# Kernel optimization log

Hardware: AMD Instinct MI355X
Metric: run time of the kernel (lower is better)

## Reference

```python
import jax, jax.numpy as jnp
import numpy as np


def _gnn_layer(feat, W, b, src, dst, n_nodes):
    # edge-wise: gather src feats -> Linear -> scatter-sum at dst
    m = feat @ W + b                                   # [N, out]
    agg = jax.ops.segment_sum(m[src], dst, num_segments=n_nodes)  # [N, out]
    # concat aggregated messages with self-transformed features -> 2*out
    return jnp.concatenate([agg, m], axis=-1)


def setup_inputs() -> dict:
    key = jax.random.key(0)
    ks = jax.random.split(key, 6)
    N, E, D_IN, D_OUT = 50000, 800000, 128, 128
    features = jax.random.normal(ks[0], (N, D_IN), dtype=jnp.float32)
    src = jax.random.randint(ks[1], (E,), 0, N, dtype=jnp.int32)
    dst = jax.random.randint(ks[2], (E,), 0, N, dtype=jnp.int32)
    W1 = jax.random.normal(ks[3], (D_IN, D_OUT), dtype=jnp.float32) / np.sqrt(D_IN)
    b1 = jnp.zeros((D_OUT,), dtype=jnp.float32)
    W2 = jax.random.normal(ks[4], (2 * D_OUT, D_OUT), dtype=jnp.float32) / np.sqrt(2 * D_OUT)
    b2 = jnp.zeros((D_OUT,), dtype=jnp.float32)
    return {"features": features, "src": src, "dst": dst,
            "W1": W1, "b1": b1, "W2": W2, "b2": b2}


def reference(features, src, dst, W1, b1, W2, b2):
    n_nodes = features.shape[0]
    feat = _gnn_layer(features, W1, b1, src, dst, n_nodes)  # [N, 2*out]
    feat = _gnn_layer(feat, W2, b2, src, dst, n_nodes)      # [N, 2*out]
    return feat
```

## Files before the change

### kernel.cpp

```cpp
#include <hip/hip_runtime.h>


#define D 128
#define CBLK 256
#define DCAP 6144

typedef __attribute__((ext_vector_type(8))) short short8;
typedef __attribute__((ext_vector_type(4))) float float4v;
typedef unsigned short ushort_t;
typedef unsigned int uint_t;

static __device__ __forceinline__ ushort_t f2bf(float f) {
    uint_t u = __builtin_bit_cast(uint_t, f);
    u += 0x7FFFu + ((u >> 16) & 1u);
    return (ushort_t)(u >> 16);
}
static __device__ __forceinline__ float bfhi(uint_t u) {
    return __builtin_bit_cast(float, u & 0xFFFF0000u);
}
static __device__ __forceinline__ float bflo(uint_t u) {
    return __builtin_bit_cast(float, u << 16);
}

static __device__ __forceinline__ void gemm1_body(
    const float* __restrict__ X, const ushort_t* __restrict__ Wp,
    const float* __restrict__ bias, ushort_t* __restrict__ Ybf,
    int N, int gb)
{
    const int wave = threadIdx.x >> 6;
    const int lane = threadIdx.x & 63;
    const int quad = lane >> 4;
    const int l16  = lane & 15;
    const int r0   = gb * 64 + wave * 16;

    float4v acc[8];
    #pragma unroll
    for (int cg = 0; cg < 8; ++cg) {
        float bv = bias[cg * 16 + l16];
        float4v b4 = {bv, bv, bv, bv};
        acc[cg] = b4;
    }

    const short8* wp8 = (const short8*)Wp;

    #pragma unroll
    for (int kb = 0; kb < 4; ++kb) {
        const int k0 = kb * 32 + quad * 8;
        int row = r0 + l16;
        if (row >= N) row = N - 1;
        const float* p = &X[(size_t)row * D + k0];
        float4 x0 = *(const float4*)p;
        float4 x1 = *(const float4*)(p + 4);
        short8 a;
        a[0] = (short)f2bf(x0.x); a[1] = (short)f2bf(x0.y);
        a[2] = (short)f2bf(x0.z); a[3] = (short)f2bf(x0.w);
        a[4] = (short)f2bf(x1.x); a[5] = (short)f2bf(x1.y);
        a[6] = (short)f2bf(x1.z); a[7] = (short)f2bf(x1.w);
        #pragma unroll
        for (int cg = 0; cg < 8; ++cg) {
            short8 b = wp8[(kb * 8 + cg) * 64 + lane];
            acc[cg] = __builtin_amdgcn_mfma_f32_16x16x32_bf16(a, b, acc[cg], 0, 0, 0);
        }
    }

    const int rowb = r0 + quad * 4;
    #pragma unroll
    for (int cg = 0; cg < 8; ++cg) {
        int col = cg * 16 + l16;
        #pragma unroll
        for (int i = 0; i < 4; ++i) {
            int row = rowb + i;
            if (row < N) Ybf[(size_t)row * D + col] = f2bf(acc[cg][i]);
        }
    }
}

__global__ __launch_bounds__(256) void packw_binA(
    const float* __restrict__ W1, const float* __restrict__ W2,
    ushort_t* __restrict__ W1p, ushort_t* __restrict__ W2p,
    const int* __restrict__ dst, int* __restrict__ mat, int E, int NB)
{
    __shared__ int h[256];
    if (blockIdx.x < CBLK) {
        const int c = blockIdx.x;
        for (int i = threadIdx.x; i < NB; i += 256) h[i] = 0;
        __syncthreads();
        const int chunk = (E + CBLK - 1) / CBLK;
        int e0 = c * chunk, e1 = e0 + chunk; if (e1 > E) e1 = E;
        for (int e = e0 + threadIdx.x; e < e1; e += 256)
            atomicAdd(&h[dst[e] >> 8], 1);
        __syncthreads();
        for (int i = threadIdx.x; i < NB; i += 256)
            mat[i * CBLK + c] = h[i];
        return;
    }
    const int n1 = 4 * 8 * 64;
    const int n2 = 8 * 8 * 64;
    int t = (blockIdx.x - CBLK) * 256 + threadIdx.x;
    if (t >= n1 + n2) return;
    const float* W; ushort_t* Wp; int tt;
    if (t < n1) { W = W1; Wp = W1p; tt = t; }
    else        { W = W2; Wp = W2p; tt = t - n1; }
    int lane = tt & 63, cg = (tt >> 6) & 7, kb = tt >> 9;
    int krow = kb * 32 + (lane >> 4) * 8;
    int col  = cg * 16 + (lane & 15);
    #pragma unroll
    for (int j = 0; j < 8; ++j)
        Wp[(size_t)tt * 8 + j] = f2bf(W[(size_t)(krow + j) * D + col]);
}

__global__ __launch_bounds__(256) void binB(
    const int* __restrict__ mat, int* __restrict__ matc,
    int* __restrict__ bb, int* __restrict__ offs, int E, int N, int NB)
{
    __shared__ int s[256];
    __shared__ int ex[256];
    const int b = blockIdx.x;
    const int tid = threadIdx.x;

    int v = 0;
    if (tid < NB) {
        const int* row = &mat[tid * CBLK];
        for (int c = 0; c < CBLK; ++c) v += row[c];
    }
    s[tid] = v; __syncthreads();
    for (int o = 1; o < 256; o <<= 1) {
        int t = (tid >= o) ? s[tid - o] : 0;
        __syncthreads();
        s[tid] += t;
        __syncthreads();
    }
    ex[tid] = s[tid] - v;
    __syncthreads();
    if (b == 0) {
        if (tid < NB) bb[tid] = ex[tid];
        if (tid == 0) { bb[NB] = E; offs[N] = E; }
    }
    const int bbb = ex[b];

    int v2 = mat[b * CBLK + tid];
    __syncthreads();
    s[tid] = v2; __syncthreads();
    for (int o = 1; o < 256; o <<= 1) {
        int t = (tid >= o) ? s[tid - o] : 0;
        __syncthreads();
        s[tid] += t;
        __syncthreads();
    }
    matc[b * CBLK + tid] = bbb + s[tid] - v2;
}

__global__ __launch_bounds__(256) void binC_gemm1(
    const int* __restrict__ src, const int* __restrict__ dst,
    const int* __restrict__ matc, int2* __restrict__ tmp, int E, int NB,
    const float* __restrict__ X, const ushort_t* __restrict__ Wp,
    const float* __restrict__ bias, ushort_t* __restrict__ Ybf, int N)
{
    __shared__ int base[256];
    __shared__ int lcnt[256];
    if (blockIdx.x < CBLK) {
        const int c = blockIdx.x;
        for (int i = threadIdx.x; i < NB; i += 256) {
            base[i] = matc[i * CBLK + c];
            lcnt[i] = 0;
        }
        __syncthreads();
        const int chunk = (E + CBLK - 1) / CBLK;
        int e0 = c * chunk, e1 = e0 + chunk; if (e1 > E) e1 = E;
        for (int e = e0 + threadIdx.x; e < e1; e += 256) {
            int d = dst[e];
            int b = d >> 8;
            int p = base[b] + atomicAdd(&lcnt[b], 1);
            int2 pr; pr.x = d; pr.y = src[e];
            tmp[p] = pr;
        }
        return;
    }
    gemm1_body(X, Wp, bias, Ybf, N, blockIdx.x - CBLK);
}

__global__ __launch_bounds__(256) void binD_gemm1(
    const int2* __restrict__ tmp, const int* __restrict__ bb,
    int* __restrict__ offs, int* __restrict__ bsrc, int N, int NB,
    const float* __restrict__ X, const ushort_t* __restrict__ Wp,
    const float* __restrict__ bias, ushort_t* __restrict__ Ybf, int gb0)
{
    __shared__ int hist[256];
    __shared__ int foff[256];
    __shared__ int cntf[256];
    __shared__ int outS[DCAP];
    if (blockIdx.x >= (uint_t)NB) {
        gemm1_body(X, Wp, bias, Ybf, N, blockIdx.x - NB + gb0);
        return;
    }
    const int b = blockIdx.x;
    const int tid = threadIdx.x;
    const int beg = bb[b], end = bb[b + 1];
    const int cnt = end - beg;
    const int n0 = b << 8;

    hist[tid] = 0;
    __syncthreads();
    for (int i = tid; i < cnt; i += 256)
        atomicAdd(&hist[tmp[beg + i].x & 255], 1);
    __syncthreads();
    int v = hist[tid];
    __syncthreads();
    hist[tid] = v; __syncthreads();
    for (int o = 1; o < 256; o <<= 1) {
        int t = (tid >= o) ? hist[tid - o] : 0;
        __syncthreads();
        hist[tid] += t;
        __syncthreads();
    }
    foff[tid] = hist[tid] - v;
    cntf[tid] = 0;
    __syncthreads();

    int node = n0 + tid;
    if (node < N) offs[node] = beg + foff[tid];

    if (cnt <= DCAP) {
        for (int i = tid; i < cnt; i += 256) {
            int2 p = tmp[beg + i];
            int f = p.x & 255;
            int pos = foff[f] + atomicAdd(&cntf[f], 1);
            outS[pos] = p.y;
        }
        __syncthreads();
        for (int i = tid; i < cnt; i += 256)
            bsrc[beg + i] = outS[i];
    } else {
        for (int i = tid; i < cnt; i += 256) {
            int2 p = tmp[beg + i];
            int f = p.x & 255;
            int pos = foff[f] + atomicAdd(&cntf[f], 1);
            bsrc[beg + pos] = p.y;
        }
    }
}

__global__ __launch_bounds__(256) void gemm2_mfma(
    const ushort_t* __restrict__ A0, const ushort_t* __restrict__ A1,
    const ushort_t* __restrict__ Wp, const float* __restrict__ bias,
    float* __restrict__ Yf, ushort_t* __restrict__ Ybf, int N)
{
    const int wave = threadIdx.x >> 6;
    const int lane = threadIdx.x & 63;
    const int quad = lane >> 4;
    const int l16  = lane & 15;
    const int r0   = blockIdx.x * 64 + wave * 16;

    float4v acc[8];
    #pragma unroll
    for (int cg = 0; cg < 8; ++cg) {
        float bv = bias[cg * 16 + l16];
        float4v b4 = {bv, bv, bv, bv};
        acc[cg] = b4;
    }

    const short8* wp8 = (const short8*)Wp;

    #pragma unroll
    for (int kb = 0; kb < 8; ++kb) {
        const ushort_t* __restrict__ A = (kb < 4) ? A0 : A1;
        const int k0 = (kb & 3) * 32 + quad * 8;
        int row = r0 + l16;
        if (row >= N) row = N - 1;
        short8 a = *(const short8*)&A[(size_t)row * D + k0];
        #pragma unroll
        for (int cg = 0; cg < 8; ++cg) {
            short8 b = wp8[(kb * 8 + cg) * 64 + lane];
            acc[cg] = __builtin_amdgcn_mfma_f32_16x16x32_bf16(a, b, acc[cg], 0, 0, 0);
        }
    }

    const int rowb = r0 + quad * 4;
    #pragma unroll
    for (int cg = 0; cg < 8; ++cg) {
        int col = cg * 16 + l16;
        #pragma unroll
        for (int i = 0; i < 4; ++i) {
            int row = rowb + i;
            if (row < N) {
                float v = acc[cg][i];
                Yf[(size_t)row * 256 + col] = v;
                Ybf[(size_t)row * D + col] = f2bf(v);
            }
        }
    }
}

__global__ __launch_bounds__(256) void gather_bf(
    const ushort_t* __restrict__ msg,
    const int* __restrict__ offs, const int* __restrict__ bsrc,
    ushort_t* __restrict__ aggB,
    float* __restrict__ aggF,
    int N)
{
    int node = (blockIdx.x * 256 + threadIdx.x) >> 6;
    int lane = threadIdx.x & 63;
    if (node >= N) return;
    const int quad = lane >> 4;
    const int c16  = lane & 15;
    int beg = offs[node], end = offs[node + 1];

    float ax[4] = {0.f, 0.f, 0.f, 0.f};
    float ay[4] = {0.f, 0.f, 0.f, 0.f};
    const uint4* mp = (const uint4*)msg;

    for (int base = beg; base < end; base += 64) {
        int cnt = end - base; if (cnt > 64) cnt = 64;
        int sidx = bsrc[base + (lane < cnt ? lane : cnt - 1)];
        for (int j0 = 0; j0 < cnt; j0 += 16) {
            #pragma unroll
            for (int t = 0; t < 4; ++t) {
                int e  = j0 + t * 4 + quad;
                int ec = (e < cnt) ? e : cnt - 1;
                int s  = __shfl(sidx, ec, 64);
                uint4 u = mp[(size_t)s * 16 + c16];
                if (e < cnt) {
                    ax[0] += bflo(u.x); ay[0] += bfhi(u.x);
                    ax[1] += bflo(u.y); ay[1] += bfhi(u.y);
                    ax[2] += bflo(u.z); ay[2] += bfhi(u.z);
                    ax[3] += bflo(u.w); ay[3] += bfhi(u.w);
                }
            }
        }
    }

    #pragma unroll
    for (int k = 0; k < 4; ++k) {
        ax[k] += __shfl_xor(ax[k], 16, 64);
        ax[k] += __shfl_xor(ax[k], 32, 64);
        ay[k] += __shfl_xor(ay[k], 16, 64);
        ay[k] += __shfl_xor(ay[k], 32, 64);
    }

    if (quad == 0) {
        if (aggB) {
            uint4 o;
            o.x = (uint_t)f2bf(ax[0]) | ((uint_t)f2bf(ay[0]) << 16);
            o.y = (uint_t)f2bf(ax[1]) | ((uint_t)f2bf(ay[1]) << 16);
            o.z = (uint_t)f2bf(ax[2]) | ((uint_t)f2bf(ay[2]) << 16);
            o.w = (uint_t)f2bf(ax[3]) | ((uint_t)f2bf(ay[3]) << 16);
            ((uint4*)aggB)[(size_t)node * 16 + c16] = o;
        } else {
            float4 w0 = {ax[0], ay[0], ax[1], ay[1]};
            float4 w1 = {ax[2], ay[2], ax[3], ay[3]};
            float* p = &aggF[(size_t)node * 256 + c16 * 8];
            *(float4*)p = w0;
            *(float4*)(p + 4) = w1;
        }
    }
}

extern "C" void kernel_launch(void* const* d_in, const int* in_sizes, int n_in,
                              void* d_out, int out_size, void* d_ws, size_t ws_size,
                              hipStream_t stream) {
    const float* features = (const float*)d_in[0];
    const int*   src      = (const int*)d_in[1];
    const int*   dst      = (const int*)d_in[2];
    const float* W1       = (const float*)d_in[3];
    const float* b1       = (const float*)d_in[4];
    const float* W2       = (const float*)d_in[5];
    const float* b2       = (const float*)d_in[6];
    float* out = (float*)d_out;

    const int N = in_sizes[0] / D;
    const int E = in_sizes[1];
    const int NB = (N + 255) >> 8;

    ushort_t* m1bf   = (ushort_t*)d_ws;
    ushort_t* agg1bf = m1bf + (size_t)N * D;
    ushort_t* m2bf   = agg1bf + (size_t)N * D;
    ushort_t* W1p    = m2bf + (size_t)N * D;
    ushort_t* W2p    = W1p + 16384;
    int*  mat  = (int*)(W2p + 32768);
    int*  matc = mat + (size_t)NB * CBLK;
    int*  bb   = matc + (size_t)NB * CBLK;
    int*  offs = bb + NB + 1;
    int2* tmp  = (int2*)(offs + N + 1);
    int*  bsrc = (int*)(tmp + (size_t)E);

    const int gemmBlocks = (N + 63) / 64;
    const int gbA = (gemmBlocks * 3) / 5;

    packw_binA<<<CBLK + 24, 256, 0, stream>>>(W1, W2, W1p, W2p, dst, mat, E, NB);
    binB<<<NB, 256, 0, stream>>>(mat, matc, bb, offs, E, N, NB);
    binC_gemm1<<<CBLK + gbA, 256, 0, stream>>>(src, dst, matc, tmp, E, NB,
                                               features, W1p, b1, m1bf, N);
    binD_gemm1<<<NB + (gemmBlocks - gbA), 256, 0, stream>>>(
        tmp, bb, offs, bsrc, N, NB, features, W1p, b1, m1bf, gbA);
    gather_bf<<<(N * 64 + 255) / 256, 256, 0, stream>>>(m1bf, offs, bsrc,
                                                        agg1bf, nullptr, N);
    gemm2_mfma<<<gemmBlocks, 256, 0, stream>>>(agg1bf, m1bf, W2p, b2,
                                               out + D, m2bf, N);
    gather_bf<<<(N * 64 + 255) / 256, 256, 0, stream>>>(m2bf, offs, bsrc,
                                                        nullptr, out, N);
}
```

Measured before the change: 205.5 us.

## Split bin-D scatter across four blocks per bin and double bin-C chunk count

Each destination bin in the second-pass sort is now handled by four blocks. Every block redundantly builds per-quarter histograms so it can compute its own starting offsets, then scatters only its quarter of the edges directly to global memory; the shared-memory staging buffer is dropped. CBLK goes from 256 to 512 so the counting and binning passes use more chunks, with binB scanning pairs to match, and the GEMM split between the two fused kernels is rebalanced. The aim is more parallelism in the sort phases, at the cost of each bin's tmp segment being read four extra times for the histograms and of uncoalesced global writes.

Result: slower. 215.4 us (+4.9%).

```diff
diff --git a/kernel.cpp b/kernel.cpp
--- a/kernel.cpp
+++ b/kernel.cpp
@@ -2,8 +2,7 @@
 
 
 #define D 128
-#define CBLK 256
-#define DCAP 6144
+#define CBLK 512
 
 typedef __attribute__((ext_vector_type(8))) short short8;
 typedef __attribute__((ext_vector_type(4))) float float4v;
@@ -138,16 +137,20 @@
     }
     const int bbb = ex[b];
 
-    int v2 = mat[b * CBLK + tid];
+    int v0 = mat[b * CBLK + 2 * tid];
+    int v1 = mat[b * CBLK + 2 * tid + 1];
+    int pair = v0 + v1;
     __syncthreads();
-    s[tid] = v2; __syncthreads();
+    s[tid] = pair; __syncthreads();
     for (int o = 1; o < 256; o <<= 1) {
         int t = (tid >= o) ? s[tid - o] : 0;
         __syncthreads();
         s[tid] += t;
         __syncthreads();
     }
-    matc[b * CBLK + tid] = bbb + s[tid] - v2;
+    int base = s[tid] - pair;
+    matc[b * CBLK + 2 * tid]     = bbb + base;
+    matc[b * CBLK + 2 * tid + 1] = bbb + base + v0;
 }
 
 __global__ __launch_bounds__(256) void binC_gemm1(
@@ -185,58 +188,59 @@
     const float* __restrict__ X, const ushort_t* __restrict__ Wp,
     const float* __restrict__ bias, ushort_t* __restrict__ Ybf, int gb0)
 {
-    __shared__ int hist[256];
+    __shared__ int h[4][256];
+    __shared__ int sc[256];
     __shared__ int foff[256];
     __shared__ int cntf[256];
-    __shared__ int outS[DCAP];
-    if (blockIdx.x >= (uint_t)NB) {
-        gemm1_body(X, Wp, bias, Ybf, N, blockIdx.x - NB + gb0);
+    if (blockIdx.x >= (uint_t)(NB * 4)) {
+        gemm1_body(X, Wp, bias, Ybf, N, blockIdx.x - NB * 4 + gb0);
         return;
     }
-    const int b = blockIdx.x;
+    const int b   = blockIdx.x >> 2;
+    const int sub = blockIdx.x & 3;
     const int tid = threadIdx.x;
     const int beg = bb[b], end = bb[b + 1];
     const int cnt = end - beg;
     const int n0 = b << 8;
 
-    hist[tid] = 0;
+    h[0][tid] = 0; h[1][tid] = 0; h[2][tid] = 0; h[3][tid] = 0;
     __syncthreads();
-    for (int i = tid; i < cnt; i += 256)
-        atomicAdd(&hist[tmp[beg + i].x & 255], 1);
+
+    const int c1 = cnt >> 2, c2 = cnt >> 1, c3 = cnt - (cnt >> 2);
+    for (int i = tid; i < cnt; i += 256) {
+        int f = tmp[beg + i].x & 255;
+        int q = (i >= c1) + (i >= c2) + (i >= c3);
+        atomicAdd(&h[q][f], 1);
+    }
     __syncthreads();
-    int v = hist[tid];
+
+    int v = h[0][tid] + h[1][tid] + h[2][tid] + h[3][tid];
+    int start = 0;
+    if (sub > 0) start += h[0][tid];
+    if (sub > 1) start += h[1][tid];
+    if (sub > 2) start += h[2][tid];
+    cntf[tid] = start;
+
+    sc[tid] = v; __syncthreads();
+    for (int o = 1; o < 256; o <<= 1) {
+        int t = (tid >= o) ? sc[tid - o] : 0;
+        __syncthreads();
+        sc[tid] += t;
+        __syncthreads();
+    }
+    foff[tid] = sc[tid] - v;
     __syncthreads();
-    hist[tid] = v; __syncthreads();
-    for (int o = 1; o < 256; o <<= 1) {
-        int t = (tid >= o) ? hist[tid - o] : 0;
-        __syncthreads();
-        hist[tid] += t;
-        __syncthreads();
-    }
-    foff[tid] = hist[tid] - v;
-    cntf[tid] = 0;
-    __syncthreads();
 
     int node = n0 + tid;
-    if (node < N) offs[node] = beg + foff[tid];
-
-    if (cnt <= DCAP) {
-        for (int i = tid; i < cnt; i += 256) {
-            int2 p = tmp[beg + i];
-            int f = p.x & 255;
-            int pos = foff[f] + atomicAdd(&cntf[f], 1);
-            outS[pos] = p.y;
-        }
-        __syncthreads();
-        for (int i = tid; i < cnt; i += 256)
-            bsrc[beg + i] = outS[i];
-    } else {
-        for (int i = tid; i < cnt; i += 256) {
-            int2 p = tmp[beg + i];
-            int f = p.x & 255;
-            int pos = foff[f] + atomicAdd(&cntf[f], 1);
-            bsrc[beg + pos] = p.y;
-        }
+    if (sub == 0 && node < N) offs[node] = beg + foff[tid];
+
+    const int s0 = (sub == 0) ? 0  : ((sub == 1) ? c1 : ((sub == 2) ? c2 : c3));
+    const int s1 = (sub == 0) ? c1 : ((sub == 1) ? c2 : ((sub == 2) ? c3 : cnt));
+    for (int i = s0 + tid; i < s1; i += 256) {
+        int2 p = tmp[beg + i];
+        int f = p.x & 255;
+        int pos = foff[f] + atomicAdd(&cntf[f], 1);
+        bsrc[beg + pos] = p.y;
     }
 }
 
@@ -384,13 +388,13 @@
     int*  bsrc = (int*)(tmp + (size_t)E);
 
     const int gemmBlocks = (N + 63) / 64;
-    const int gbA = (gemmBlocks * 3) / 5;
+    const int gbA = gemmBlocks / 2;
 
     packw_binA<<<CBLK + 24, 256, 0, stream>>>(W1, W2, W1p, W2p, dst, mat, E, NB);
     binB<<<NB, 256, 0, stream>>>(mat, matc, bb, offs, E, N, NB);
     binC_gemm1<<<CBLK + gbA, 256, 0, stream>>>(src, dst, matc, tmp, E, NB,
                                                features, W1p, b1, m1bf, N);
-    binD_gemm1<<<NB + (gemmBlocks - gbA), 256, 0, stream>>>(
+    binD_gemm1<<<NB * 4 + (gemmBlocks - gbA), 256, 0, stream>>>(
         tmp, bb, offs, bsrc, N, NB, features, W1p, b1, m1bf, gbA);
     gather_bf<<<(N * 64 + 255) / 256, 256, 0, stream>>>(m1bf, offs, bsrc,
                                                         agg1bf, nullptr, N);
```

## Split layer-1 gather and overlap its second half with first-half GEMM2

Applied to the files above, without the earlier changes.

Splits the first gather into two node halves. The second half of the gather runs in the same launch as GEMM2 over the first half of the rows, which only needs the already-finished first-half aggregates. The remaining GEMM2 rows run in a separate launch afterwards. This co-schedules the memory-bound gather with MFMA work to hide tail effects, at the cost of one extra kernel launch and more code.

New measurement: 220.5 us. 1.07x slower.

```diff
diff --git a/kernel.cpp b/kernel.cpp
--- a/kernel.cpp
+++ b/kernel.cpp
@@ -75,181 +75,16 @@
     }
 }
 
-__global__ __launch_bounds__(256) void packw_binA(
-    const float* __restrict__ W1, const float* __restrict__ W2,
-    ushort_t* __restrict__ W1p, ushort_t* __restrict__ W2p,
-    const int* __restrict__ dst, int* __restrict__ mat, int E, int NB)
-{
-    __shared__ int h[256];
-    if (blockIdx.x < CBLK) {
-        const int c = blockIdx.x;
-        for (int i = threadIdx.x; i < NB; i += 256) h[i] = 0;
-        __syncthreads();
-        const int chunk = (E + CBLK - 1) / CBLK;
-        int e0 = c * chunk, e1 = e0 + chunk; if (e1 > E) e1 = E;
-        for (int e = e0 + threadIdx.x; e < e1; e += 256)
-            atomicAdd(&h[dst[e] >> 8], 1);
-        __syncthreads();
-        for (int i = threadIdx.x; i < NB; i += 256)
-            mat[i * CBLK + c] = h[i];
-        return;
-    }
-    const int n1 = 4 * 8 * 64;
-    const int n2 = 8 * 8 * 64;
-    int t = (blockIdx.x - CBLK) * 256 + threadIdx.x;
-    if (t >= n1 + n2) return;
-    const float* W; ushort_t* Wp; int tt;
-    if (t < n1) { W = W1; Wp = W1p; tt = t; }
-    else        { W = W2; Wp = W2p; tt = t - n1; }
-    int lane = tt & 63, cg = (tt >> 6) & 7, kb = tt >> 9;
-    int krow = kb * 32 + (lane >> 4) * 8;
-    int col  = cg * 16 + (lane & 15);
-    #pragma unroll
-    for (int j = 0; j < 8; ++j)
-        Wp[(size_t)tt * 8 + j] = f2bf(W[(size_t)(krow + j) * D + col]);
-}
-
-__global__ __launch_bounds__(256) void binB(
-    const int* __restrict__ mat, int* __restrict__ matc,
-    int* __restrict__ bb, int* __restrict__ offs, int E, int N, int NB)
-{
-    __shared__ int s[256];
-    __shared__ int ex[256];
-    const int b = blockIdx.x;
-    const int tid = threadIdx.x;
-
-    int v = 0;
-    if (tid < NB) {
-        const int* row = &mat[tid * CBLK];
-        for (int c = 0; c < CBLK; ++c) v += row[c];
-    }
-    s[tid] = v; __syncthreads();
-    for (int o = 1; o < 256; o <<= 1) {
-        int t = (tid >= o) ? s[tid - o] : 0;
-        __syncthreads();
-        s[tid] += t;
-        __syncthreads();
-    }
-    ex[tid] = s[tid] - v;
-    __syncthreads();
-    if (b == 0) {
-        if (tid < NB) bb[tid] = ex[tid];
-        if (tid == 0) { bb[NB] = E; offs[N] = E; }
-    }
-    const int bbb = ex[b];
-
-    int v2 = mat[b * CBLK + tid];
-    __syncthreads();
-    s[tid] = v2; __syncthreads();
-    for (int o = 1; o < 256; o <<= 1) {
-        int t = (tid >= o) ? s[tid - o] : 0;
-        __syncthreads();
-        s[tid] += t;
-        __syncthreads();
-    }
-    matc[b * CBLK + tid] = bbb + s[tid] - v2;
-}
-
-__global__ __launch_bounds__(256) void binC_gemm1(
-    const int* __restrict__ src, const int* __restrict__ dst,
-    const int* __restrict__ matc, int2* __restrict__ tmp, int E, int NB,
-    const float* __restrict__ X, const ushort_t* __restrict__ Wp,
-    const float* __restrict__ bias, ushort_t* __restrict__ Ybf, int N)
-{
-    __shared__ int base[256];
-    __shared__ int lcnt[256];
-    if (blockIdx.x < CBLK) {
-        const int c = blockIdx.x;
-        for (int i = threadIdx.x; i < NB; i += 256) {
-            base[i] = matc[i * CBLK + c];
-            lcnt[i] = 0;
-        }
-        __syncthreads();
-        const int chunk = (E + CBLK - 1) / CBLK;
-        int e0 = c * chunk, e1 = e0 + chunk; if (e1 > E) e1 = E;
-        for (int e = e0 + threadIdx.x; e < e1; e += 256) {
-            int d = dst[e];
-            int b = d >> 8;
-            int p = base[b] + atomicAdd(&lcnt[b], 1);
-            int2 pr; pr.x = d; pr.y = src[e];
-            tmp[p] = pr;
-        }
-        return;
-    }
-    gemm1_body(X, Wp, bias, Ybf, N, blockIdx.x - CBLK);
-}
-
-__global__ __launch_bounds__(256) void binD_gemm1(
-    const int2* __restrict__ tmp, const int* __restrict__ bb,
-    int* __restrict__ offs, int* __restrict__ bsrc, int N, int NB,
-    const float* __restrict__ X, const ushort_t* __restrict__ Wp,
-    const float* __restrict__ bias, ushort_t* __restrict__ Ybf, int gb0)
-{
-    __shared__ int hist[256];
-    __shared__ int foff[256];
-    __shared__ int cntf[256];
-    __shared__ int outS[DCAP];
-    if (blockIdx.x >= (uint_t)NB) {
-        gemm1_body(X, Wp, bias, Ybf, N, blockIdx.x - NB + gb0);
-        return;
-    }
-    const int b = blockIdx.x;
-    const int tid = threadIdx.x;
-    const int beg = bb[b], end = bb[b + 1];
-    const int cnt = end - beg;
-    const int n0 = b << 8;
-
-    hist[tid] = 0;
-    __syncthreads();
-    for (int i = tid; i < cnt; i += 256)
-        atomicAdd(&hist[tmp[beg + i].x & 255], 1);
-    __syncthreads();
-    int v = hist[tid];
-    __syncthreads();
-    hist[tid] = v; __syncthreads();
-    for (int o = 1; o < 256; o <<= 1) {
-        int t = (tid >= o) ? hist[tid - o] : 0;
-        __syncthreads();
-        hist[tid] += t;
-        __syncthreads();
-    }
-    foff[tid] = hist[tid] - v;
-    cntf[tid] = 0;
-    __syncthreads();
-
-    int node = n0 + tid;
-    if (node < N) offs[node] = beg + foff[tid];
-
-    if (cnt <= DCAP) {
-        for (int i = tid; i < cnt; i += 256) {
-            int2 p = tmp[beg + i];
-            int f = p.x & 255;
-            int pos = foff[f] + atomicAdd(&cntf[f], 1);
-            outS[pos] = p.y;
-        }
-        __syncthreads();
-        for (int i = tid; i < cnt; i += 256)
-            bsrc[beg + i] = outS[i];
-    } else {
-        for (int i = tid; i < cnt; i += 256) {
-            int2 p = tmp[beg + i];
-            int f = p.x & 255;
-            int pos = foff[f] + atomicAdd(&cntf[f], 1);
-            bsrc[beg + pos] = p.y;
-        }
-    }
-}
-
-__global__ __launch_bounds__(256) void gemm2_mfma(
+static __device__ __forceinline__ void gemm2_body(
     const ushort_t* __restrict__ A0, const ushort_t* __restrict__ A1,
     const ushort_t* __restrict__ Wp, const float* __restrict__ bias,
-    float* __restrict__ Yf, ushort_t* __restrict__ Ybf, int N)
+    float* __restrict__ Yf, ushort_t* __restrict__ Ybf, int N, int gb)
 {
     const int wave = threadIdx.x >> 6;
     const int lane = threadIdx.x & 63;
     const int quad = lane >> 4;
     const int l16  = lane & 15;
-    const int r0   = blockIdx.x * 64 + wave * 16;
+    const int r0   = gb * 64 + wave * 16;
 
     float4v acc[8];
     #pragma unroll
@@ -291,16 +126,12 @@
     }
 }
 
-__global__ __launch_bounds__(256) void gather_bf(
+static __device__ __forceinline__ void gather_body(
     const ushort_t* __restrict__ msg,
     const int* __restrict__ offs, const int* __restrict__ bsrc,
-    ushort_t* __restrict__ aggB,
-    float* __restrict__ aggF,
-    int N)
-{
-    int node = (blockIdx.x * 256 + threadIdx.x) >> 6;
-    int lane = threadIdx.x & 63;
-    if (node >= N) return;
+    ushort_t* __restrict__ aggB, float* __restrict__ aggF, int node)
+{
+    const int lane = threadIdx.x & 63;
     const int quad = lane >> 4;
     const int c16  = lane & 15;
     int beg = offs[node], end = offs[node + 1];
@@ -355,6 +186,216 @@
     }
 }
 
+__global__ __launch_bounds__(256) void packw_binA(
+    const float* __restrict__ W1, const float* __restrict__ W2,
+    ushort_t* __restrict__ W1p, ushort_t* __restrict__ W2p,
+    const int* __restrict__ dst, int* __restrict__ mat, int E, int NB)
+{
+    __shared__ int h[256];
+    if (blockIdx.x < CBLK) {
+        const int c = blockIdx.x;
+        for (int i = threadIdx.x; i < NB; i += 256) h[i] = 0;
+        __syncthreads();
+        const int chunk = (E + CBLK - 1) / CBLK;
+        int e0 = c * chunk, e1 = e0 + chunk; if (e1 > E) e1 = E;
+        for (int e = e0 + threadIdx.x; e < e1; e += 256)
+            atomicAdd(&h[dst[e] >> 8], 1);
+        __syncthreads();
+        for (int i = threadIdx.x; i < NB; i += 256)
+            mat[i * CBLK + c] = h[i];
+        return;
+    }
+    const int n1 = 4 * 8 * 64;
+    const int n2 = 8 * 8 * 64;
+    int t = (blockIdx.x - CBLK) * 256 + threadIdx.x;
+    if (t >= n1 + n2) return;
+    const float* W; ushort_t* Wp; int tt;
+    if (t < n1) { W = W1; Wp = W1p; tt = t; }
+    else        { W = W2; Wp = W2p; tt = t - n1; }
+    int lane = tt & 63, cg = (tt >> 6) & 7, kb = tt >> 9;
+    int krow = kb * 32 + (lane >> 4) * 8;
+    int col  = cg * 16 + (lane & 15);
+    #pragma unroll
+    for (int j = 0; j < 8; ++j)
+        Wp[(size_t)tt * 8 + j] = f2bf(W[(size_t)(krow + j) * D + col]);
+}
+
+__global__ __launch_bounds__(256) void binB(
+    const int* __restrict__ mat, int* __restrict__ matc,
+    int* __restrict__ bb, int* __restrict__ offs, int E, int N, int NB)
+{
+    __shared__ int s[256];
+    __shared__ int ex[256];
+    const int b = blockIdx.x;
+    const int tid = threadIdx.x;
+
+    int v = 0;
+    if (tid < NB) {
+        const int* row = &mat[tid * CBLK];
+        for (int c = 0; c < CBLK; ++c) v += row[c];
+    }
+    s[tid] = v; __syncthreads();
+    for (int o = 1; o < 256; o <<= 1) {
+        int t = (tid >= o) ? s[tid - o] : 0;
+        __syncthreads();
+        s[tid] += t;
+        __syncthreads();
+    }
+    ex[tid] = s[tid] - v;
+    __syncthreads();
+    if (b == 0) {
+        if (tid < NB) bb[tid] = ex[tid];
+        if (tid == 0) { bb[NB] = E; offs[N] = E; }
+    }
+    const int bbb = ex[b];
+
+    int v2 = mat[b * CBLK + tid];
+    __syncthreads();
+    s[tid] = v2; __syncthreads();
+    for (int o = 1; o < 256; o <<= 1) {
+        int t = (tid >= o) ? s[tid - o] : 0;
+        __syncthreads();
+        s[tid] += t;
+        __syncthreads();
+    }
+    matc[b * CBLK + tid] = bbb + s[tid] - v2;
+}
+
+__global__ __launch_bounds__(256) void binC_gemm1(
+    const int* __restrict__ src, const int* __restrict__ dst,
+    const int* __restrict__ matc, int2* __restrict__ tmp, int E, int NB,
+    const float* __restrict__ X, const ushort_t* __restrict__ Wp,
+    const float* __restrict__ bias, ushort_t* __restrict__ Ybf, int N)
+{
+    __shared__ int base[256];
+    __shared__ int lcnt[256];
+    if (blockIdx.x < CBLK) {
+        const int c = blockIdx.x;
+        for (int i = threadIdx.x; i < NB; i += 256) {
+            base[i] = matc[i * CBLK + c];
+            lcnt[i] = 0;
+        }
+        __syncthreads();
+        const int chunk = (E + CBLK - 1) / CBLK;
+        int e0 = c * chunk, e1 = e0 + chunk; if (e1 > E) e1 = E;
+        for (int e = e0 + threadIdx.x; e < e1; e += 256) {
+            int d = dst[e];
+            int b = d >> 8;
+            int p = base[b] + atomicAdd(&lcnt[b], 1);
+            int2 pr; pr.x = d; pr.y = src[e];
+            tmp[p] = pr;
+        }
+        return;
+    }
+    gemm1_body(X, Wp, bias, Ybf, N, blockIdx.x - CBLK);
+}
+
+__global__ __launch_bounds__(256) void binD_gemm1(
+    const int2* __restrict__ tmp, const int* __restrict__ bb,
+    int* __restrict__ offs, int* __restrict__ bsrc, int N, int NB,
+    const float* __restrict__ X, const ushort_t* __restrict__ Wp,
+    const float* __restrict__ bias, ushort_t* __restrict__ Ybf, int gb0)
+{
+    __shared__ int hist[256];
+    __shared__ int foff[256];
+    __shared__ int cntf[256];
+    __shared__ int outS[DCAP];
+    if (blockIdx.x >= (uint_t)NB) {
+        gemm1_body(X, Wp, bias, Ybf, N, blockIdx.x - NB + gb0);
+        return;
+    }
+    const int b = blockIdx.x;
+    const int tid = threadIdx.x;
+    const int beg = bb[b], end = bb[b + 1];
+    const int cnt = end - beg;
+    const int n0 = b << 8;
+
+    hist[tid] = 0;
+    __syncthreads();
+    for (int i = tid; i < cnt; i += 256)
+        atomicAdd(&hist[tmp[beg + i].x & 255], 1);
+    __syncthreads();
+    int v = hist[tid];
+    __syncthreads();
+    hist[tid] = v; __syncthreads();
+    for (int o = 1; o < 256; o <<= 1) {
+        int t = (tid >= o) ? hist[tid - o] : 0;
+        __syncthreads();
+        hist[tid] += t;
+        __syncthreads();
+    }
+    foff[tid] = hist[tid] - v;
+    cntf[tid] = 0;
+    __syncthreads();
+
+    int node = n0 + tid;
+    if (node < N) offs[node] = beg + foff[tid];
+
+    if (cnt <= DCAP) {
+        for (int i = tid; i < cnt; i += 256) {
+            int2 p = tmp[beg + i];
+            int f = p.x & 255;
+            int pos = foff[f] + atomicAdd(&cntf[f], 1);
+            outS[pos] = p.y;
+        }
+        __syncthreads();
+        for (int i = tid; i < cnt; i += 256)
+            bsrc[beg + i] = outS[i];
+    } else {
+        for (int i = tid; i < cnt; i += 256) {
+            int2 p = tmp[beg + i];
+            int f = p.x & 255;
+            int pos = foff[f] + atomicAdd(&cntf[f], 1);
+            bsrc[beg + pos] = p.y;
+        }
+    }
+}
+
+__global__ __launch_bounds__(256) void gather1_a(
+    const ushort_t* __restrict__ msg,
+    const int* __restrict__ offs, const int* __restrict__ bsrc,
+    ushort_t* __restrict__ aggB, int Nh)
+{
+    int node = (blockIdx.x * 256 + threadIdx.x) >> 6;
+    if (node >= Nh) return;
+    gather_body(msg, offs, bsrc, aggB, nullptr, node);
+}
+
+__global__ __launch_bounds__(256) void gather1b_gemm2a(
+    const ushort_t* __restrict__ msg,
+    const int* __restrict__ offs, const int* __restrict__ bsrc,
+    ushort_t* __restrict__ aggB, int Nh, int N, int GB,
+    const ushort_t* __restrict__ A0, const ushort_t* __restrict__ Wp,
+    const float* __restrict__ bias, float* __restrict__ Yf,
+    ushort_t* __restrict__ Ybf)
+{
+    if ((int)blockIdx.x < GB) {
+        int node = Nh + (int)((blockIdx.x * 256 + threadIdx.x) >> 6);
+        if (node >= N) return;
+        gather_body(msg, offs, bsrc, aggB, nullptr, node);
+        return;
+    }
+    gemm2_body(A0, msg, Wp, bias, Yf, Ybf, N, blockIdx.x - GB);
+}
+
+__global__ __launch_bounds__(256) void gemm2_b(
+    const ushort_t* __restrict__ A0, const ushort_t* __restrict__ A1,
+    const ushort_t* __restrict__ Wp, const float* __restrict__ bias,
+    float* __restrict__ Yf, ushort_t* __restrict__ Ybf, int N, int gb0)
+{
+    gemm2_body(A0, A1, Wp, bias, Yf, Ybf, N, blockIdx.x + gb0);
+}
+
+__global__ __launch_bounds__(256) void gather2(
+    const ushort_t* __restrict__ msg,
+    const int* __restrict__ offs, const int* __restrict__ bsrc,
+    float* __restrict__ aggF, int N)
+{
+    int node = (blockIdx.x * 256 + threadIdx.x) >> 6;
+    if (node >= N) return;
+    gather_body(msg, offs, bsrc, nullptr, aggF, node);
+}
+
 extern "C" void kernel_launch(void* const* d_in, const int* in_sizes, int n_in,
                               void* d_out, int out_size, void* d_ws, size_t ws_size,
                               hipStream_t stream) {
@@ -386,16 +427,22 @@
     const int gemmBlocks = (N + 63) / 64;
     const int gbA = (gemmBlocks * 3) / 5;
 
+    const int Nh = ((N / 2) + 63) & ~63;
+    const int gH = Nh / 64;
+    const int g1aBlocks = (Nh * 64 + 255) / 256;
+    const int g1bBlocks = ((N - Nh) * 64 + 255) / 256;
+
     packw_binA<<<CBLK + 24, 256, 0, stream>>>(W1, W2, W1p, W2p, dst, mat, E, NB);
     binB<<<NB, 256, 0, stream>>>(mat, matc, bb, offs, E, N, NB);
     binC_gemm1<<<CBLK + gbA, 256, 0, stream>>>(src, dst, matc, tmp, E, NB,
                                                features, W1p, b1, m1bf, N);
     binD_gemm1<<<NB + (gemmBlocks - gbA), 256, 0, stream>>>(
         tmp, bb, offs, bsrc, N, NB, features, W1p, b1, m1bf, gbA);
-    gather_bf<<<(N * 64 + 255) / 256, 256, 0, stream>>>(m1bf, offs, bsrc,
-                                                        agg1bf, nullptr, N);
-    gemm2_mfma<<<gemmBlocks, 256, 0, stream>>>(agg1bf, m1bf, W2p, b2,
-                                               out + D, m2bf, N);
-    gather_bf<<<(N * 64 + 255) / 256, 256, 0, stream>>>(m2bf, offs, bsrc,
-                                                        nullptr, out, N);
-}
+    gather1_a<<<g1aBlocks, 256, 0, stream>>>(m1bf, offs, bsrc, agg1bf, Nh);
+    gather1b_gemm2a<<<g1bBlocks + gH, 256, 0, stream>>>(
+        m1bf, offs, bsrc, agg1bf, Nh, N, g1bBlocks,
+        agg1bf, W2p, b2, out + D, m2bf);
+    gemm2_b<<<gemmBlocks - gH, 256, 0, stream>>>(agg1bf, m1bf, W2p, b2,
+                                                 out + D, m2bf, N, gH);
+    gather2<<<(N * 64 + 255) / 256, 256, 0, stream>>>(m2bf, offs, bsrc, out, N);
+}
```
